# Optimization experiments

Hardware: AMD Instinct MI355X
Metric: run time of the kernel (lower is better)

## Reference

```python
import jax, jax.numpy as jnp
import numpy as np

EMBED = 1024
HEADS = 16
HEAD_DIM = EMBED // HEADS


def setup_inputs() -> dict:
    key = jax.random.key(0)
    k1, k2, k3, k4, k5 = jax.random.split(key, 5)
    N, S = 2, 2048
    values = jax.random.normal(k1, (N, S, EMBED), dtype=jnp.float32)
    keys = jax.random.normal(k2, (N, S, EMBED), dtype=jnp.float32)
    query = jax.random.normal(k3, (N, S, EMBED), dtype=jnp.float32)
    mask = jnp.ones((N, 1, S, S), dtype=jnp.int32)
    # fc_out: Linear(heads*head_dim, embed_size) with bias; torch stores W as [out, in]
    W_out = jax.random.normal(k4, (EMBED, EMBED), dtype=jnp.float32) / np.sqrt(EMBED)
    b_out = jax.random.normal(k5, (EMBED,), dtype=jnp.float32) * 0.01
    return {"values": values, "keys": keys, "query": query, "mask": mask,
            "W_out": W_out, "b_out": b_out}


def reference(values, keys, query, mask, W_out, b_out):
    N, S, E = query.shape
    H, D = HEADS, HEAD_DIM
    # NOTE: source module never applies its q/k/v Linear layers (bug preserved).
    v = values.reshape(N, S, H, D)
    k = keys.reshape(N, S, H, D)
    q = query.reshape(N, S, H, D)
    energy = jnp.einsum('nqhd,nkhd->nhqk', q, k)  # [N,H,S,S]
    energy = jnp.where(mask == 0, jnp.float32(-1e20), energy)
    # non-standard scale: sqrt(embed_size), faithful to source
    attn = jax.nn.softmax(energy / jnp.sqrt(jnp.float32(E)), axis=3)
    out = jnp.einsum('nhql,nlhd->nqhd', attn, v).reshape(N, S, H * D)
    return out @ W_out.T + b_out
```

## Files before the change

kernel.cpp:

```cpp
#include <hip/hip_runtime.h>
#include <stdint.h>

#define S_LEN 2048
#define EMB 1024
#define NHEADS 16
#define HD 64
#define LOG2E 1.4426950408889634f

typedef __bf16 bf16x8 __attribute__((ext_vector_type(8)));
typedef float f32x4 __attribute__((ext_vector_type(4)));
typedef unsigned short u16;

#define MFMA16(a, b, c) __builtin_amdgcn_mfma_f32_16x16x32_bf16(a, b, c, 0, 0, 0)
#define GLOAD_LDS16(gp, lp)                                        \
  __builtin_amdgcn_global_load_lds(                                \
      (const __attribute__((address_space(1))) unsigned int*)(gp), \
      (__attribute__((address_space(3))) unsigned int*)(lp), 16, 0, 0)

__device__ __forceinline__ u16 bf16r(float x) {
  union { float f; unsigned int u; } c; c.f = x;
  unsigned int u = c.u + 0x7fffu + ((c.u >> 16) & 1u);
  return (u16)(u >> 16);
}

__device__ __forceinline__ unsigned int cvt_pk_bf16(float lo, float hi) {
  unsigned int r;
  asm("v_cvt_pk_bf16_f32 %0, %1, %2" : "=v"(r) : "v"(lo), "v"(hi));
  return r;
}

__device__ __forceinline__ float fexp2(float x) {
  float r;
  asm("v_exp_f32 %0, %1" : "=v"(r) : "v"(x));
  return r;
}

__global__ __launch_bounds__(256) void prep_kernel(
    const float* __restrict__ values, const float* __restrict__ keys,
    const float* __restrict__ W, const int* __restrict__ mask,
    u16* __restrict__ vt, u16* __restrict__ kb, u16* __restrict__ wb,
    unsigned char* __restrict__ fl2) {
  __shared__ u16 tile[64][65];
  __shared__ int s_ok[4];
  int b = blockIdx.x;
  int t = threadIdx.x;
  if (b < 1024) {
    int st = b & 31, h = (b >> 5) & 15, n = b >> 9;
    int s0 = st * 64;
    int d = t & 63, r4 = t >> 6;
#pragma unroll
    for (int i = 0; i < 16; ++i) {
      int s = r4 + i * 4;
      float x = values[(size_t)(n * S_LEN + s0 + s) * EMB + h * HD + d];
      tile[s][d] = bf16r(x);
    }
    __syncthreads();
#pragma unroll
    for (int i = 0; i < 16; ++i) {
      int dd = r4 + i * 4;
      vt[(size_t)((n * NHEADS + h) * HD + dd) * S_LEN + s0 + d] = tile[d][dd];
    }
  } else if (b < 2048) {
    int idx = (b - 1024) * 256 + t;
    const float4* in4 = (const float4*)keys;
    ushort4* out4 = (ushort4*)kb;
#pragma unroll
    for (int j = 0; j < 4; ++j) {
      float4 v = in4[idx + j * 262144];
      ushort4 o;
      o.x = bf16r(v.x); o.y = bf16r(v.y); o.z = bf16r(v.z); o.w = bf16r(v.w);
      out4[idx + j * 262144] = o;
    }
  } else if (b < 2304) {
    int idx = (b - 2048) * 256 + t;
    const float4* in4 = (const float4*)W;
    ushort4* out4 = (ushort4*)wb;
#pragma unroll
    for (int j = 0; j < 4; ++j) {
      float4 v = in4[idx + j * 65536];
      ushort4 o;
      o.x = bf16r(v.x); o.y = bf16r(v.y); o.z = bf16r(v.z); o.w = bf16r(v.w);
      out4[idx + j * 65536] = o;
    }
  } else {
    int idx = b - 2304;
    int kt = idx & 31, qt = (idx >> 5) & 15, n = idx >> 9;
    int qr = t >> 1, c8 = t & 1;
    const int4* mp = (const int4*)(mask + (size_t)n * S_LEN * S_LEN +
                                   (size_t)(qt * 128 + qr) * S_LEN + kt * 64) + c8 * 8;
    int ok = 1;
#pragma unroll
    for (int i = 0; i < 8; ++i) {
      int4 m = mp[i];
      ok &= (m.x != 0) & (m.y != 0) & (m.z != 0) & (m.w != 0);
    }
    ok = __all(ok);
    if ((t & 63) == 0) s_ok[t >> 6] = ok;
    __syncthreads();
    if (t == 0) fl2[idx] = (unsigned char)(s_ok[0] & s_ok[1] & s_ok[2] & s_ok[3]);
  }
}

__global__ __launch_bounds__(256) void attn_kernel(
    const float* __restrict__ query, const u16* __restrict__ kbuf,
    const u16* __restrict__ vt, const int* __restrict__ mask,
    const unsigned char* __restrict__ fl2, u16* __restrict__ ob) {
  __shared__ __align__(16) unsigned char kl[2][8192];
  __shared__ __align__(16) unsigned char vl[2][8192];
  __shared__ __align__(16) u16 pl[4][2][16][72];

  int b = blockIdx.x;
  b = (b & 7) * 64 + (b >> 3);
  int qt = b & 15, h = (b >> 4) & 15, n = b >> 8;
  int t = threadIdx.x, w = t >> 6, l = t & 63, l16 = l & 15, g = l >> 4;
  int q0w = qt * 128 + w * 32;

  bf16x8 aq[2][2];
#pragma unroll
  for (int u = 0; u < 2; ++u)
#pragma unroll
    for (int hh = 0; hh < 2; ++hh) {
      const float* qp = query + (size_t)(n * S_LEN + q0w + u * 16 + l16) * EMB +
                        h * HD + hh * 32 + g * 8;
      float4 f0 = *(const float4*)qp;
      float4 f1 = *(const float4*)(qp + 4);
      union { bf16x8 v; unsigned int u32[4]; } qq;
      qq.u32[0] = cvt_pk_bf16(f0.x * 0.03125f, f0.y * 0.03125f);
      qq.u32[1] = cvt_pk_bf16(f0.z * 0.03125f, f0.w * 0.03125f);
      qq.u32[2] = cvt_pk_bf16(f1.x * 0.03125f, f1.y * 0.03125f);
      qq.u32[3] = cvt_pk_bf16(f1.z * 0.03125f, f1.w * 0.03125f);
      aq[u][hh] = qq.v;
    }

  f32x4 zero4 = {0.f, 0.f, 0.f, 0.f};
  f32x4 acc[2][4];
  float lrun[2] = {0.f, 0.f}, mrun[2] = {0.f, 0.f}, mL[2] = {0.f, 0.f};
#pragma unroll
  for (int u = 0; u < 2; ++u)
#pragma unroll
    for (int db = 0; db < 4; ++db) acc[u][db] = zero4;

  int row_s = t >> 3, cc = t & 7;
  int sc = cc ^ (row_s & 7);
  const u16* gk0 = kbuf + (size_t)(n * S_LEN + row_s) * EMB + h * HD + sc * 8;
  const u16* gv0 = vt + (size_t)((n * NHEADS + h) * HD + row_s) * S_LEN + sc * 8;

  auto stage = [&](int kt, int nb) {
    const u16* gk = gk0 + (size_t)kt * 64 * EMB;
    const u16* gv = gv0 + kt * 64;
    GLOAD_LDS16(gk, kl[nb] + (w * 64) * 16);
    GLOAD_LDS16(gk + 32 * EMB, kl[nb] + (256 + w * 64) * 16);
    GLOAD_LDS16(gv, vl[nb] + (w * 64) * 16);
    GLOAD_LDS16(gv + 32 * S_LEN, vl[nb] + (256 + w * 64) * 16);
  };

  stage(0, 0);
  __syncthreads();

  for (int kt = 0; kt < S_LEN / 64; ++kt) {
    int cur = kt & 1;
    if (kt + 1 < S_LEN / 64) stage(kt + 1, cur ^ 1);
    const unsigned char* kc = kl[cur];
    const unsigned char* vc = vl[cur];

    f32x4 sf[2][4];
    __builtin_amdgcn_s_setprio(1);
#pragma unroll
    for (int kb = 0; kb < 4; ++kb) {
      int row = kb * 16 + l16;
      const unsigned char* kr = kc + row * 128;
      int sw = (row & 7) << 4;
      bf16x8 bk0 = *(const bf16x8*)(kr + ((g * 16) ^ sw));
      bf16x8 bk1 = *(const bf16x8*)(kr + ((64 + g * 16) ^ sw));
#pragma unroll
      for (int u = 0; u < 2; ++u) {
        f32x4 z = zero4;
        z = MFMA16(bk0, aq[u][0], z);
        z = MFMA16(bk1, aq[u][1], z);
        sf[u][kb] = z;
      }
    }
    __builtin_amdgcn_s_setprio(0);

    unsigned char fflag = fl2[((n * 16 + qt) * 32) + kt];
    if (!fflag) {
#pragma unroll
      for (int u = 0; u < 2; ++u) {
        const int* mrow = mask + (size_t)n * S_LEN * S_LEN +
                          (size_t)(q0w + u * 16 + l16) * S_LEN + kt * 64 + g * 4;
#pragma unroll
        for (int kb = 0; kb < 4; ++kb) {
          int4 mm = *(const int4*)(mrow + kb * 16);
          if (mm.x == 0) sf[u][kb][0] = -30.f;
          if (mm.y == 0) sf[u][kb][1] = -30.f;
          if (mm.z == 0) sf[u][kb][2] = -30.f;
          if (mm.w == 0) sf[u][kb][3] = -30.f;
        }
      }
    }

#pragma unroll
    for (int u = 0; u < 2; ++u) {
      float lmax = sf[u][0][0];
#pragma unroll
      for (int kb = 0; kb < 4; ++kb)
#pragma unroll
        for (int r = 0; r < 4; ++r) lmax = fmaxf(lmax, sf[u][kb][r]);
      if (!__all(lmax <= mrun[u] + 8.f)) {
        float rmax = fmaxf(lmax, __shfl_xor(lmax, 16));
        rmax = fmaxf(rmax, __shfl_xor(rmax, 32));
        float Mn = fmaxf(mrun[u], rmax);
        float corr = fexp2((mrun[u] - Mn) * LOG2E);
        mrun[u] = Mn;
        mL[u] = Mn * LOG2E;
        lrun[u] *= corr;
#pragma unroll
        for (int r = 0; r < 4; ++r) {
          float ca = __shfl(corr, (l & 48) + (g << 2) + r);
#pragma unroll
          for (int db = 0; db < 4; ++db) acc[u][db][r] *= ca;
        }
      }
      float p[4][4];
#pragma unroll
      for (int kb = 0; kb < 4; ++kb)
#pragma unroll
        for (int r = 0; r < 4; ++r)
          p[kb][r] = fexp2(fmaf(sf[u][kb][r], LOG2E, -mL[u]));
      float s01 = (p[0][0] + p[0][1]) + (p[0][2] + p[0][3]);
      float s23 = (p[1][0] + p[1][1]) + (p[1][2] + p[1][3]);
      float s45 = (p[2][0] + p[2][1]) + (p[2][2] + p[2][3]);
      float s67 = (p[3][0] + p[3][1]) + (p[3][2] + p[3][3]);
      lrun[u] += (s01 + s23) + (s45 + s67);
#pragma unroll
      for (int kb = 0; kb < 4; ++kb) {
        uint2 pw;
        pw.x = cvt_pk_bf16(p[kb][0], p[kb][1]);
        pw.y = cvt_pk_bf16(p[kb][2], p[kb][3]);
        *(uint2*)(&pl[w][u][l16][kb * 16 + g * 4]) = pw;
      }
    }
    __builtin_amdgcn_wave_barrier();

    __builtin_amdgcn_s_setprio(1);
#pragma unroll
    for (int hh = 0; hh < 2; ++hh) {
      bf16x8 ap0 = *(const bf16x8*)(&pl[w][0][l16][hh * 32 + g * 8]);
      bf16x8 ap1 = *(const bf16x8*)(&pl[w][1][l16][hh * 32 + g * 8]);
#pragma unroll
      for (int db = 0; db < 4; ++db) {
        int d = db * 16 + l16;
        bf16x8 bv = *(const bf16x8*)(vc + d * 128 + ((hh * 64 + g * 16) ^ ((d & 7) << 4)));
        acc[0][db] = MFMA16(ap0, bv, acc[0][db]);
        acc[1][db] = MFMA16(ap1, bv, acc[1][db]);
      }
    }
    __builtin_amdgcn_s_setprio(0);

    __syncthreads();
  }

#pragma unroll
  for (int u = 0; u < 2; ++u) {
    float s = lrun[u];
    s += __shfl_xor(s, 16);
    s += __shfl_xor(s, 32);
    float rinv[4];
#pragma unroll
    for (int r = 0; r < 4; ++r) {
      float sr = __shfl(s, (l & 48) + (g << 2) + r);
      rinv[r] = 1.f / sr;
    }
#pragma unroll
    for (int db = 0; db < 4; ++db)
#pragma unroll
      for (int r = 0; r < 4; ++r) {
        int qg = q0w + u * 16 + (g << 2) + r;
        ob[(size_t)(n * S_LEN + qg) * EMB + h * HD + db * 16 + l16] =
            bf16r(acc[u][db][r] * rinv[r]);
      }
  }
}

__global__ __launch_bounds__(256) void proj_kernel(
    const u16* __restrict__ A, const u16* __restrict__ Bt,
    const float* __restrict__ bias, float* __restrict__ C) {
  __shared__ __align__(16) unsigned char al[2][16384];
  __shared__ __align__(16) unsigned char bl[2][16384];
  int bm = blockIdx.x, bn = blockIdx.y;
  int t = threadIdx.x, w = t >> 6, l = t & 63;
  int l16 = l & 15, g = l >> 4;
  int wm = w >> 1, wn = w & 1;
  f32x4 zero4 = {0.f, 0.f, 0.f, 0.f};
  f32x4 acc[4][4];
#pragma unroll
  for (int m = 0; m < 4; ++m)
#pragma unroll
    for (int nn = 0; nn < 4; ++nn) acc[m][nn] = zero4;
  int row_s = t >> 3, cc = t & 7;
  int sc = cc ^ (row_s & 7);
  const u16* ga0 = A + (size_t)(bm * 128 + row_s) * EMB + sc * 8;
  const u16* gb0 = Bt + (size_t)(bn * 128 + row_s) * EMB + sc * 8;

  auto stage = [&](int ks, int nb) {
#pragma unroll
    for (int i = 0; i < 4; ++i) {
      GLOAD_LDS16(ga0 + (size_t)i * 32 * EMB + ks * 64, al[nb] + (i * 256 + w * 64) * 16);
      GLOAD_LDS16(gb0 + (size_t)i * 32 * EMB + ks * 64, bl[nb] + (i * 256 + w * 64) * 16);
    }
  };

  stage(0, 0);
  __syncthreads();

  for (int ks = 0; ks < 16; ++ks) {
    int cur = ks & 1;
    if (ks + 1 < 16) stage(ks + 1, cur ^ 1);
    __builtin_amdgcn_s_setprio(1);
#pragma unroll
    for (int hh = 0; hh < 2; ++hh) {
      bf16x8 af[4], bfr[4];
#pragma unroll
      for (int m = 0; m < 4; ++m) {
        int row = wm * 64 + m * 16 + l16;
        af[m] = *(const bf16x8*)(al[cur] + row * 128 + ((hh * 64 + g * 16) ^ ((row & 7) << 4)));
      }
#pragma unroll
      for (int nn = 0; nn < 4; ++nn) {
        int row = wn * 64 + nn * 16 + l16;
        bfr[nn] = *(const bf16x8*)(bl[cur] + row * 128 + ((hh * 64 + g * 16) ^ ((row & 7) << 4)));
      }
#pragma unroll
      for (int m = 0; m < 4; ++m)
#pragma unroll
        for (int nn = 0; nn < 4; ++nn) acc[m][nn] = MFMA16(af[m], bfr[nn], acc[m][nn]);
    }
    __builtin_amdgcn_s_setprio(0);
    __syncthreads();
  }
#pragma unroll
  for (int nn = 0; nn < 4; ++nn) {
    int j = bn * 128 + wn * 64 + nn * 16 + l16;
    float bj = bias[j];
#pragma unroll
    for (int m = 0; m < 4; ++m) {
      int i0 = bm * 128 + wm * 64 + m * 16 + g * 4;
#pragma unroll
      for (int r = 0; r < 4; ++r) C[(size_t)(i0 + r) * EMB + j] = acc[m][nn][r] + bj;
    }
  }
}

extern "C" void kernel_launch(void* const* d_in, const int* in_sizes, int n_in,
                              void* d_out, int out_size, void* d_ws, size_t ws_size,
                              hipStream_t stream) {
  const float* values = (const float*)d_in[0];
  const float* keys = (const float*)d_in[1];
  const float* query = (const float*)d_in[2];
  const int* mask = (const int*)d_in[3];
  const float* W = (const float*)d_in[4];
  const float* bias = (const float*)d_in[5];
  float* out = (float*)d_out;

  u16* kb = (u16*)d_ws;
  u16* vt = kb + 4194304;
  u16* ob = vt + 4194304;
  u16* wb = ob + 4194304;
  unsigned char* fl2 = (unsigned char*)(wb + 1048576);

  prep_kernel<<<3328, 256, 0, stream>>>(values, keys, W, mask, vt, kb, wb, fl2);
  attn_kernel<<<512, 256, 0, stream>>>(query, kb, vt, mask, fl2, ob);
  proj_kernel<<<dim3(32, 8), 256, 0, stream>>>(ob, wb, bias, out);
}
```

Baseline: 100.5 us.

## Keep softmax probabilities in registers via permuted V layout and halve query tile

The V-transpose prep now writes keys in a permuted order that matches the MFMA output layout. The attention kernel can then pack P straight into bf16 A-operands from registers instead of round-tripping through LDS with a wave barrier. Each wave also handles 16 query rows instead of 32, which doubles the grid to 1024 blocks and allows occupancy hint 4 for better latency hiding. The cost is twice as many blocks streaming the same K/V tiles, so global and L2 traffic per query is higher and each K/V LDS load is reused half as much.

```diff
diff --git a/kernel.cpp b/kernel.cpp
--- a/kernel.cpp
+++ b/kernel.cpp
@@ -33,6 +33,11 @@
   float r;
   asm("v_exp_f32 %0, %1" : "=v"(r) : "v"(x));
   return r;
+}
+
+__device__ __forceinline__ int kperm(int k) {
+  int kb = (k >> 4) & 3, g = (k >> 2) & 3, r = k & 3;
+  return (kb >> 1) * 32 + g * 8 + (kb & 1) * 4 + r;
 }
 
 __global__ __launch_bounds__(256) void prep_kernel(
@@ -55,10 +60,11 @@
       tile[s][d] = bf16r(x);
     }
     __syncthreads();
+    int sp = s0 + kperm(d);
 #pragma unroll
     for (int i = 0; i < 16; ++i) {
       int dd = r4 + i * 4;
-      vt[(size_t)((n * NHEADS + h) * HD + dd) * S_LEN + s0 + d] = tile[d][dd];
+      vt[(size_t)((n * NHEADS + h) * HD + dd) * S_LEN + sp] = tile[d][dd];
     }
   } else if (b < 2048) {
     int idx = (b - 1024) * 256 + t;
@@ -101,44 +107,38 @@
   }
 }
 
-__global__ __launch_bounds__(256) void attn_kernel(
+__global__ __launch_bounds__(256, 4) void attn_kernel(
     const float* __restrict__ query, const u16* __restrict__ kbuf,
     const u16* __restrict__ vt, const int* __restrict__ mask,
     const unsigned char* __restrict__ fl2, u16* __restrict__ ob) {
   __shared__ __align__(16) unsigned char kl[2][8192];
   __shared__ __align__(16) unsigned char vl[2][8192];
-  __shared__ __align__(16) u16 pl[4][2][16][72];
 
   int b = blockIdx.x;
-  b = (b & 7) * 64 + (b >> 3);
-  int qt = b & 15, h = (b >> 4) & 15, n = b >> 8;
+  b = (b & 7) * 128 + (b >> 3);
+  int qt = b & 31, h = (b >> 5) & 15, n = b >> 9;
   int t = threadIdx.x, w = t >> 6, l = t & 63, l16 = l & 15, g = l >> 4;
-  int q0w = qt * 128 + w * 32;
-
-  bf16x8 aq[2][2];
-#pragma unroll
-  for (int u = 0; u < 2; ++u)
-#pragma unroll
-    for (int hh = 0; hh < 2; ++hh) {
-      const float* qp = query + (size_t)(n * S_LEN + q0w + u * 16 + l16) * EMB +
-                        h * HD + hh * 32 + g * 8;
-      float4 f0 = *(const float4*)qp;
-      float4 f1 = *(const float4*)(qp + 4);
-      union { bf16x8 v; unsigned int u32[4]; } qq;
-      qq.u32[0] = cvt_pk_bf16(f0.x * 0.03125f, f0.y * 0.03125f);
-      qq.u32[1] = cvt_pk_bf16(f0.z * 0.03125f, f0.w * 0.03125f);
-      qq.u32[2] = cvt_pk_bf16(f1.x * 0.03125f, f1.y * 0.03125f);
-      qq.u32[3] = cvt_pk_bf16(f1.z * 0.03125f, f1.w * 0.03125f);
-      aq[u][hh] = qq.v;
-    }
+  int q0w = qt * 64 + w * 16;
+
+  bf16x8 aq[2];
+#pragma unroll
+  for (int hh = 0; hh < 2; ++hh) {
+    const float* qp = query + (size_t)(n * S_LEN + q0w + l16) * EMB + h * HD + hh * 32 + g * 8;
+    float4 f0 = *(const float4*)qp;
+    float4 f1 = *(const float4*)(qp + 4);
+    union { bf16x8 v; unsigned int u32[4]; } qq;
+    qq.u32[0] = cvt_pk_bf16(f0.x * 0.03125f, f0.y * 0.03125f);
+    qq.u32[1] = cvt_pk_bf16(f0.z * 0.03125f, f0.w * 0.03125f);
+    qq.u32[2] = cvt_pk_bf16(f1.x * 0.03125f, f1.y * 0.03125f);
+    qq.u32[3] = cvt_pk_bf16(f1.z * 0.03125f, f1.w * 0.03125f);
+    aq[hh] = qq.v;
+  }
 
   f32x4 zero4 = {0.f, 0.f, 0.f, 0.f};
-  f32x4 acc[2][4];
-  float lrun[2] = {0.f, 0.f}, mrun[2] = {0.f, 0.f}, mL[2] = {0.f, 0.f};
-#pragma unroll
-  for (int u = 0; u < 2; ++u)
-#pragma unroll
-    for (int db = 0; db < 4; ++db) acc[u][db] = zero4;
+  f32x4 acc[4];
+  float lrun = 0.f, mrun = 0.f, mL = 0.f;
+#pragma unroll
+  for (int db = 0; db < 4; ++db) acc[db] = zero4;
 
   int row_s = t >> 3, cc = t & 7;
   int sc = cc ^ (row_s & 7);
@@ -163,7 +163,7 @@
     const unsigned char* kc = kl[cur];
     const unsigned char* vc = vl[cur];
 
-    f32x4 sf[2][4];
+    f32x4 sf[4];
     __builtin_amdgcn_s_setprio(1);
 #pragma unroll
     for (int kb = 0; kb < 4; ++kb) {
@@ -172,114 +172,101 @@
       int sw = (row & 7) << 4;
       bf16x8 bk0 = *(const bf16x8*)(kr + ((g * 16) ^ sw));
       bf16x8 bk1 = *(const bf16x8*)(kr + ((64 + g * 16) ^ sw));
-#pragma unroll
-      for (int u = 0; u < 2; ++u) {
-        f32x4 z = zero4;
-        z = MFMA16(bk0, aq[u][0], z);
-        z = MFMA16(bk1, aq[u][1], z);
-        sf[u][kb] = z;
-      }
+      f32x4 z = zero4;
+      z = MFMA16(bk0, aq[0], z);
+      z = MFMA16(bk1, aq[1], z);
+      sf[kb] = z;
     }
     __builtin_amdgcn_s_setprio(0);
 
-    unsigned char fflag = fl2[((n * 16 + qt) * 32) + kt];
+    unsigned char fflag = fl2[((n * 16 + (qt >> 1)) * 32) + kt];
     if (!fflag) {
-#pragma unroll
-      for (int u = 0; u < 2; ++u) {
-        const int* mrow = mask + (size_t)n * S_LEN * S_LEN +
-                          (size_t)(q0w + u * 16 + l16) * S_LEN + kt * 64 + g * 4;
-#pragma unroll
-        for (int kb = 0; kb < 4; ++kb) {
-          int4 mm = *(const int4*)(mrow + kb * 16);
-          if (mm.x == 0) sf[u][kb][0] = -30.f;
-          if (mm.y == 0) sf[u][kb][1] = -30.f;
-          if (mm.z == 0) sf[u][kb][2] = -30.f;
-          if (mm.w == 0) sf[u][kb][3] = -30.f;
-        }
-      }
-    }
-
-#pragma unroll
-    for (int u = 0; u < 2; ++u) {
-      float lmax = sf[u][0][0];
-#pragma unroll
-      for (int kb = 0; kb < 4; ++kb)
-#pragma unroll
-        for (int r = 0; r < 4; ++r) lmax = fmaxf(lmax, sf[u][kb][r]);
-      if (!__all(lmax <= mrun[u] + 8.f)) {
-        float rmax = fmaxf(lmax, __shfl_xor(lmax, 16));
-        rmax = fmaxf(rmax, __shfl_xor(rmax, 32));
-        float Mn = fmaxf(mrun[u], rmax);
-        float corr = fexp2((mrun[u] - Mn) * LOG2E);
-        mrun[u] = Mn;
-        mL[u] = Mn * LOG2E;
-        lrun[u] *= corr;
-#pragma unroll
-        for (int r = 0; r < 4; ++r) {
-          float ca = __shfl(corr, (l & 48) + (g << 2) + r);
-#pragma unroll
-          for (int db = 0; db < 4; ++db) acc[u][db][r] *= ca;
-        }
-      }
-      float p[4][4];
-#pragma unroll
-      for (int kb = 0; kb < 4; ++kb)
-#pragma unroll
-        for (int r = 0; r < 4; ++r)
-          p[kb][r] = fexp2(fmaf(sf[u][kb][r], LOG2E, -mL[u]));
-      float s01 = (p[0][0] + p[0][1]) + (p[0][2] + p[0][3]);
-      float s23 = (p[1][0] + p[1][1]) + (p[1][2] + p[1][3]);
-      float s45 = (p[2][0] + p[2][1]) + (p[2][2] + p[2][3]);
-      float s67 = (p[3][0] + p[3][1]) + (p[3][2] + p[3][3]);
-      lrun[u] += (s01 + s23) + (s45 + s67);
+      const int* mrow = mask + (size_t)n * S_LEN * S_LEN +
+                        (size_t)(q0w + l16) * S_LEN + kt * 64 + g * 4;
 #pragma unroll
       for (int kb = 0; kb < 4; ++kb) {
-        uint2 pw;
-        pw.x = cvt_pk_bf16(p[kb][0], p[kb][1]);
-        pw.y = cvt_pk_bf16(p[kb][2], p[kb][3]);
-        *(uint2*)(&pl[w][u][l16][kb * 16 + g * 4]) = pw;
-      }
-    }
-    __builtin_amdgcn_wave_barrier();
+        int4 mm = *(const int4*)(mrow + kb * 16);
+        if (mm.x == 0) sf[kb][0] = -30.f;
+        if (mm.y == 0) sf[kb][1] = -30.f;
+        if (mm.z == 0) sf[kb][2] = -30.f;
+        if (mm.w == 0) sf[kb][3] = -30.f;
+      }
+    }
+
+    float lmax = sf[0][0];
+#pragma unroll
+    for (int kb = 0; kb < 4; ++kb)
+#pragma unroll
+      for (int r = 0; r < 4; ++r) lmax = fmaxf(lmax, sf[kb][r]);
+    if (!__all(lmax <= mrun + 8.f)) {
+      float rmax = fmaxf(lmax, __shfl_xor(lmax, 16));
+      rmax = fmaxf(rmax, __shfl_xor(rmax, 32));
+      float Mn = fmaxf(mrun, rmax);
+      float corr = fexp2((mrun - Mn) * LOG2E);
+      mrun = Mn;
+      mL = Mn * LOG2E;
+      lrun *= corr;
+#pragma unroll
+      for (int r = 0; r < 4; ++r) {
+        float ca = __shfl(corr, (l & 48) + (g << 2) + r);
+#pragma unroll
+        for (int db = 0; db < 4; ++db) acc[db][r] *= ca;
+      }
+    }
+    float p[4][4];
+#pragma unroll
+    for (int kb = 0; kb < 4; ++kb)
+#pragma unroll
+      for (int r = 0; r < 4; ++r)
+        p[kb][r] = fexp2(fmaf(sf[kb][r], LOG2E, -mL));
+    float s01 = (p[0][0] + p[0][1]) + (p[0][2] + p[0][3]);
+    float s23 = (p[1][0] + p[1][1]) + (p[1][2] + p[1][3]);
+    float s45 = (p[2][0] + p[2][1]) + (p[2][2] + p[2][3]);
+    float s67 = (p[3][0] + p[3][1]) + (p[3][2] + p[3][3]);
+    lrun += (s01 + s23) + (s45 + s67);
+
+    bf16x8 pa[2];
+#pragma unroll
+    for (int hh = 0; hh < 2; ++hh) {
+      union { bf16x8 v; unsigned int u32[4]; } pp;
+      pp.u32[0] = cvt_pk_bf16(p[2 * hh][0], p[2 * hh][1]);
+      pp.u32[1] = cvt_pk_bf16(p[2 * hh][2], p[2 * hh][3]);
+      pp.u32[2] = cvt_pk_bf16(p[2 * hh + 1][0], p[2 * hh + 1][1]);
+      pp.u32[3] = cvt_pk_bf16(p[2 * hh + 1][2], p[2 * hh + 1][3]);
+      pa[hh] = pp.v;
+    }
 
     __builtin_amdgcn_s_setprio(1);
 #pragma unroll
-    for (int hh = 0; hh < 2; ++hh) {
-      bf16x8 ap0 = *(const bf16x8*)(&pl[w][0][l16][hh * 32 + g * 8]);
-      bf16x8 ap1 = *(const bf16x8*)(&pl[w][1][l16][hh * 32 + g * 8]);
+    for (int hh = 0; hh < 2; ++hh)
 #pragma unroll
       for (int db = 0; db < 4; ++db) {
         int d = db * 16 + l16;
         bf16x8 bv = *(const bf16x8*)(vc + d * 128 + ((hh * 64 + g * 16) ^ ((d & 7) << 4)));
-        acc[0][db] = MFMA16(ap0, bv, acc[0][db]);
-        acc[1][db] = MFMA16(ap1, bv, acc[1][db]);
-      }
-    }
+        acc[db] = MFMA16(pa[hh], bv, acc[db]);
+      }
     __builtin_amdgcn_s_setprio(0);
 
     __syncthreads();
   }
 
-#pragma unroll
-  for (int u = 0; u < 2; ++u) {
-    float s = lrun[u];
-    s += __shfl_xor(s, 16);
-    s += __shfl_xor(s, 32);
-    float rinv[4];
+  float s = lrun;
+  s += __shfl_xor(s, 16);
+  s += __shfl_xor(s, 32);
+  float rinv[4];
+#pragma unroll
+  for (int r = 0; r < 4; ++r) {
+    float sr = __shfl(s, (l & 48) + (g << 2) + r);
+    rinv[r] = 1.f / sr;
+  }
+#pragma unroll
+  for (int db = 0; db < 4; ++db)
 #pragma unroll
     for (int r = 0; r < 4; ++r) {
-      float sr = __shfl(s, (l & 48) + (g << 2) + r);
-      rinv[r] = 1.f / sr;
-    }
-#pragma unroll
-    for (int db = 0; db < 4; ++db)
-#pragma unroll
-      for (int r = 0; r < 4; ++r) {
-        int qg = q0w + u * 16 + (g << 2) + r;
-        ob[(size_t)(n * S_LEN + qg) * EMB + h * HD + db * 16 + l16] =
-            bf16r(acc[u][db][r] * rinv[r]);
-      }
-  }
+      int qg = q0w + (g << 2) + r;
+      ob[(size_t)(n * S_LEN + qg) * EMB + h * HD + db * 16 + l16] =
+          bf16r(acc[db][r] * rinv[r]);
+    }
 }
 
 __global__ __launch_bounds__(256) void proj_kernel(
@@ -369,6 +356,6 @@
   unsigned char* fl2 = (unsigned char*)(wb + 1048576);
 
   prep_kernel<<<3328, 256, 0, stream>>>(values, keys, W, mask, vt, kb, wb, fl2);
-  attn_kernel<<<512, 256, 0, stream>>>(query, kb, vt, mask, fl2, ob);
+  attn_kernel<<<1024, 256, 0, stream>>>(query, kb, vt, mask, fl2, ob);
   proj_kernel<<<dim3(32, 8), 256, 0, stream>>>(ob, wb, bias, out);
 }
```

Measured after the change: 96.85 us. 3.6% less time.
